# Kernel tuning notes

Measured on AMD Instinct MI355X. Metric: run time of the kernel, lower is better.

## Reference

```python
import jax, jax.numpy as jnp
import numpy as np

EPS = 1e-5
D_MODEL = 64
D_STATE = 16
D_INNER = 128  # expand=2
DT_RANK = 4    # ceil(64/16)


def _inorm(x):
    # InstanceNorm2d (affine=False), NCHW, biased variance, eps=1e-5
    mu = jnp.mean(x, axis=(2, 3), keepdims=True)
    var = jnp.var(x, axis=(2, 3), keepdims=True)
    return (x - mu) * jax.lax.rsqrt(var + EPS)


def _conv2d(x, w, b=None, groups=1):
    y = jax.lax.conv_general_dilated(x, w, (1, 1), 'SAME',
        dimension_numbers=('NCHW', 'OIHW', 'NCHW'), feature_group_count=groups)
    return y if b is None else y + b[None, :, None, None]


def _layernorm(x, w, b):
    mu = jnp.mean(x, axis=-1, keepdims=True)
    var = jnp.var(x, axis=-1, keepdims=True)
    return (x - mu) * jax.lax.rsqrt(var + EPS) * w + b


def _selective_scan(u, delta, A, Bm, Cm, Dp, delta_bias):
    # u, delta: (B,d,L); A: (d,N); Bm,Cm: (B,N,L); Dp: (d,)
    delta = jax.nn.softplus(delta + delta_bias[None, :, None])
    dA = jnp.exp(jnp.einsum('bdl,dn->lbdn', delta, A))        # (L,B,d,N)
    dBu = jnp.einsum('bdl,bnl->lbdn', delta * u, Bm)          # (L,B,d,N)
    Cl = jnp.transpose(Cm, (2, 0, 1))                         # (L,B,N)
    h0 = jnp.zeros((u.shape[0], u.shape[1], A.shape[1]), u.dtype)

    def step(h, inp):
        dA_l, dBu_l, c = inp
        h = dA_l * h + dBu_l
        return h, jnp.einsum('bdn,bn->bd', h, c)

    _, ys = jax.lax.scan(step, h0, (dA, dBu, Cl))             # ys: (L,B,d)
    return jnp.transpose(ys, (1, 2, 0)) + u * Dp[None, :, None]


def _forward(x, dw3_w, dw3_b, dw5_w, dw5_b, dw7_w, dw7_b, fuse_w, fuse_b,
             in_proj_w, conv2d_w, conv2d_b, x_proj_w, dt_proj_w, dt_proj_b,
             A_log, Dp, out_norm_w, out_norm_b, out_proj_w, cf_w, cf_b):
    C = x.shape[1]
    lrelu = lambda t: jax.nn.leaky_relu(t, 0.01)
    # ---- LRGS: multi-scale depthwise convs + fuse + residual (shortcut=Identity) ----
    feats = [lrelu(_inorm(_conv2d(x, w, b, groups=C)))
             for w, b in ((dw3_w, dw3_b), (dw5_w, dw5_b), (dw7_w, dw7_b))]
    xf = _conv2d(jnp.concatenate(feats, axis=1), fuse_w, fuse_b)
    x1 = lrelu(_inorm(xf)) + x
    # ---- MC_Mamba / SS2D ----
    xh = jnp.transpose(x1, (0, 2, 3, 1))           # (B,H,W,C)
    Bn, H, W, _ = xh.shape
    xz = xh @ in_proj_w.T                          # (B,H,W,2*d_inner)
    xm, z = jnp.split(xz, 2, axis=-1)
    xm = jnp.transpose(xm, (0, 3, 1, 2))           # (B,d_inner,H,W)
    xm = jax.nn.silu(_conv2d(xm, conv2d_w, conv2d_b, groups=D_INNER))
    L = H * W
    x_flat = jnp.transpose(xm.reshape(Bn, D_INNER, L), (0, 2, 1))  # (B,L,d)
    xp = x_flat @ x_proj_w.T
    dt, Bm, Cm = jnp.split(xp, [DT_RANK, DT_RANK + D_STATE], axis=-1)
    # NOTE: faithful to source, nn.Linear applies dt_proj_b here AND it is
    # passed again as delta_bias to the scan (bias applied twice).
    dt = jnp.transpose(dt @ dt_proj_w.T + dt_proj_b, (0, 2, 1))    # (B,d,L)
    A = -jnp.exp(A_log)
    y = _selective_scan(jnp.transpose(x_flat, (0, 2, 1)), dt, A,
                        jnp.transpose(Bm, (0, 2, 1)), jnp.transpose(Cm, (0, 2, 1)),
                        Dp, dt_proj_b)
    y = jnp.transpose(y, (0, 2, 1)).reshape(Bn, H, W, D_INNER)
    y = _layernorm(y, out_norm_w, out_norm_b) * jax.nn.silu(z)
    y = y @ out_proj_w.T                           # (B,H,W,d_model)
    y = jnp.transpose(y, (0, 3, 1, 2))
    y = _inorm(_conv2d(y, cf_w, cf_b))
    return x1 + y


def setup_inputs() -> dict:
    key = jax.random.key(0)
    ks = jax.random.split(key, 12)
    B, C, H, W = 8, D_MODEL, 64, 64
    s = 0.05
    return {
        'x': jax.random.normal(ks[0], (B, C, H, W), jnp.float32),
        'dw3_w': jax.random.normal(ks[1], (C, 1, 3, 3), jnp.float32) * s,
        'dw3_b': jnp.zeros((C,), jnp.float32),
        'dw5_w': jax.random.normal(ks[2], (C, 1, 5, 5), jnp.float32) * s,
        'dw5_b': jnp.zeros((C,), jnp.float32),
        'dw7_w': jax.random.normal(ks[3], (C, 1, 7, 7), jnp.float32) * s,
        'dw7_b': jnp.zeros((C,), jnp.float32),
        'fuse_w': jax.random.normal(ks[4], (C, 3 * C, 1, 1), jnp.float32) * s,
        'fuse_b': jnp.zeros((C,), jnp.float32),
        'in_proj_w': jax.random.normal(ks[5], (2 * D_INNER, D_MODEL), jnp.float32) * s,
        'conv2d_w': jax.random.normal(ks[6], (D_INNER, 1, 3, 3), jnp.float32) * s,
        'conv2d_b': jnp.zeros((D_INNER,), jnp.float32),
        'x_proj_w': jax.random.normal(ks[7], (DT_RANK + 2 * D_STATE, D_INNER), jnp.float32) * s,
        'dt_proj_w': jax.random.uniform(ks[8], (D_INNER, DT_RANK), jnp.float32, -0.5, 0.5),
        'dt_proj_b': jnp.exp(jax.random.uniform(ks[9], (D_INNER,), jnp.float32)
                             * (np.log(0.1) - np.log(0.001)) + np.log(0.001)).astype(jnp.float32),
        'A_log': jnp.log(jnp.tile(jnp.arange(1, D_STATE + 1, dtype=jnp.float32), (D_INNER, 1))),
        'Dp': jnp.ones((D_INNER,), jnp.float32),
        'out_norm_w': jnp.ones((D_INNER,), jnp.float32),
        'out_norm_b': jnp.zeros((D_INNER,), jnp.float32),
        'out_proj_w': jax.random.normal(ks[10], (D_MODEL, D_INNER), jnp.float32) * s,
        'cf_w': jax.random.normal(ks[11], (D_MODEL, D_MODEL, 1, 1), jnp.float32) * s,
        'cf_b': jnp.zeros((D_MODEL,), jnp.float32),
    }


def reference(x, dw3_w, dw3_b, dw5_w, dw5_b, dw7_w, dw7_b, fuse_w, fuse_b,
              in_proj_w, conv2d_w, conv2d_b, x_proj_w, dt_proj_w, dt_proj_b,
              A_log, Dp, out_norm_w, out_norm_b, out_proj_w, cf_w, cf_b):
    return _forward(x, dw3_w, dw3_b, dw5_w, dw5_b, dw7_w, dw7_b, fuse_w, fuse_b,
                    in_proj_w, conv2d_w, conv2d_b, x_proj_w, dt_proj_w, dt_proj_b,
                    A_log, Dp, out_norm_w, out_norm_b, out_proj_w, cf_w, cf_b)
```

## Files before the change

kernel.cpp:

```cpp
#include <hip/hip_runtime.h>
#include <math.h>

#define NB 8
#define NC 64
#define NL 4096
#define NDI 128
#define NN 16
#define CHUNK 32
#define NKCH 128

#define OFF_FEATS 0ull
#define OFF_AC    0ull
#define OFF_BC    2097152ull
#define OFF_HINIT 4194304ull
#define OFF_XF    6291456ull
#define OFF_BMAT  6291456ull
#define OFF_CMAT  6815744ull
#define OFF_X1    8388608ull
#define OFF_XMRAW 10485760ull
#define OFF_G     10485760ull
#define OFF_Z     14680064ull
#define OFF_YC    14680064ull
#define OFF_PART  16777216ull
#define OFF_STATS 16809984ull
#define OFF_XMC   18874368ull
#define OFF_DTM   23068672ull
#define OFF_SEGP  23199744ull
#define OFF_SEGQ  23330816ull
#define OFF_SEGH  23461888ull
#define OFF_WF    27262976ull
#define OFF_NSTAT (OFF_WF + 55552ull)
#define OFF_WCOMB (OFF_WF + 58624ull)
#define WS_NEED_FLOATS (OFF_WF + 66816ull)

#define WF_DW3    0
#define WF_DW5    576
#define WF_DW7    2176
#define WF_B3     5312
#define WF_B5     5376
#define WF_B7     5440
#define WF_FUSE   5504
#define WF_FUSEB  17792
#define WF_C2W    17856
#define WF_C2B    19008
#define WF_XPW    19136
#define WF_DTW    23744
#define WF_DTB    24256
#define WF_A      24384
#define WF_DP     26432
#define WF_ONW    26560
#define WF_ONB    26688
#define WF_OPW    26816
#define WF_CFW    35008
#define WF_CFB    39104
#define WF_INPJ   39168

struct Cvt { const float* src; float* dst; int n; int op; };
struct CvtArgs { Cvt d[22]; int ncvt; const float* cfw; const float* opw; float* wcomb; };

__global__ __launch_bounds__(256) void k0_cvt(CvtArgs a){
  if ((int)blockIdx.x < a.ncvt){
    Cvt c = a.d[blockIdx.x];
    for (int i = threadIdx.x; i < c.n; i += 256){
      float v = c.src[i];
      c.dst[i] = c.op ? -expf(v) : v;
    }
  } else {
    int idx = (blockIdx.x - a.ncvt)*256 + threadIdx.x;
    int c = idx >> 7, kk = idx & 127;
    float s = 0.f;
    #pragma unroll
    for (int j=0;j<64;j++) s += a.cfw[c*64+j] * a.opw[j*128+kk];
    a.wcomb[idx] = s;
  }
}

__global__ __launch_bounds__(256) void k1_dw(const float* __restrict__ x, const float* __restrict__ wf,
                                             float* __restrict__ feats, float* __restrict__ part){
  const int half = blockIdx.x & 1, c = (blockIdx.x >> 1) & 63, b = blockIdx.x >> 7;
  const int tid = threadIdx.x;
  const int r0 = half*32;
  __shared__ float xs[38*73];
  __shared__ float red[4][6];
  for (int i = tid; i < 38*73; i += 256) xs[i] = 0.f;
  const float* xp = x + ((size_t)b*64 + c)*NL;
  float v[10];
  #pragma unroll
  for (int k=0;k<10;k++){
    int idx = tid + k*256;
    int j = idx >> 6, w = idx & 63;
    int gr = r0 - 3 + j;
    bool ok = (idx < 2432) && (gr >= 0) && (gr < 64);
    v[k] = ok ? xp[gr*64 + w] : 0.f;
  }
  float w3r[9], w5r[25], w7r[49];
  #pragma unroll
  for (int i=0;i<9;i++)  w3r[i] = wf[WF_DW3 + c*9 + i];
  #pragma unroll
  for (int i=0;i<25;i++) w5r[i] = wf[WF_DW5 + c*25 + i];
  #pragma unroll
  for (int i=0;i<49;i++) w7r[i] = wf[WF_DW7 + c*49 + i];
  float b3 = wf[WF_B3+c], b5 = wf[WF_B5+c], b7 = wf[WF_B7+c];
  __syncthreads();
  #pragma unroll
  for (int k=0;k<10;k++){
    int idx = tid + k*256;
    if (idx < 2432){
      int j = idx >> 6, w = idx & 63;
      xs[j*73 + (w+3)] = v[k];
    }
  }
  __syncthreads();
  float s3=0,q3=0,s5=0,q5=0,s7=0,q7=0;
  float* f3 = feats + ((size_t)b*192 + c) * NL + r0*64;
  float* f5 = f3 + (size_t)64*NL;
  float* f7 = f3 + (size_t)128*NL;
  #pragma unroll
  for (int g=0; g<2; g++){
    int p = g*1024 + tid*4;
    int lh = p >> 6, w0 = p & 63;
    float a3[4], a5[4], a7[4];
    #pragma unroll
    for (int i=0;i<4;i++){ a3[i]=b3; a5[i]=b5; a7[i]=b7; }
    #pragma unroll
    for (int dy=0; dy<7; dy++){
      float s[10];
      #pragma unroll
      for (int j=0;j<10;j++) s[j] = xs[(lh+dy)*73 + w0 + j];
      #pragma unroll
      for (int dx=0;dx<7;dx++){
        float wv = w7r[dy*7+dx];
        #pragma unroll
        for (int i=0;i<4;i++) a7[i] += s[dx+i]*wv;
      }
      if (dy>=1 && dy<=5){
        #pragma unroll
        for (int dx=0;dx<5;dx++){
          float wv = w5r[(dy-1)*5+dx];
          #pragma unroll
          for (int i=0;i<4;i++) a5[i] += s[dx+1+i]*wv;
        }
      }
      if (dy>=2 && dy<=4){
        #pragma unroll
        for (int dx=0;dx<3;dx++){
          float wv = w3r[(dy-2)*3+dx];
          #pragma unroll
          for (int i=0;i<4;i++) a3[i] += s[dx+2+i]*wv;
        }
      }
    }
    *(float4*)(f3+p) = make_float4(a3[0],a3[1],a3[2],a3[3]);
    *(float4*)(f5+p) = make_float4(a5[0],a5[1],a5[2],a5[3]);
    *(float4*)(f7+p) = make_float4(a7[0],a7[1],a7[2],a7[3]);
    #pragma unroll
    for (int i=0;i<4;i++){
      s3+=a3[i]; q3+=a3[i]*a3[i];
      s5+=a5[i]; q5+=a5[i]*a5[i];
      s7+=a7[i]; q7+=a7[i]*a7[i];
    }
  }
  int wid = tid>>6, lane = tid&63;
  float v6[6]={s3,q3,s5,q5,s7,q7};
  #pragma unroll
  for (int j=0;j<6;j++){
    float t = v6[j];
    #pragma unroll
    for (int o=32;o>0;o>>=1) t += __shfl_down(t,o);
    if (!lane) red[wid][j]=t;
  }
  __syncthreads();
  if (tid < 3){
    float su = red[0][tid*2]+red[1][tid*2]+red[2][tid*2]+red[3][tid*2];
    float sq = red[0][tid*2+1]+red[1][tid*2+1]+red[2][tid*2+1]+red[3][tid*2+1];
    size_t k = (size_t)(b*192 + tid*64 + c)*4 + half*2;
    part[k]   = su;
    part[k+1] = sq;
  }
}

__global__ __launch_bounds__(256) void k2_fuse(const float* __restrict__ feats, const float* __restrict__ npart,
                                               const float* __restrict__ wf, float* __restrict__ xf){
  int og = blockIdx.x >> 8, rem = blockIdx.x & 255;
  int b = rem >> 5, pt = rem & 31;
  int jslot = threadIdx.x >> 5, pxslot = threadIdx.x & 31;
  __shared__ float wlds2[192][44];
  __shared__ float xs[32][128];
  __shared__ float msl[192], rsl[192];
  for (int i = threadIdx.x; i < 192; i += 256){
    const float* pp = npart + (size_t)(b*192+i)*4;
    float su = pp[0]+pp[2], sq = pp[1]+pp[3];
    float m = su*(1.f/NL);
    msl[i] = m;
    rsl[i] = rsqrtf(sq*(1.f/NL) - m*m + 1e-5f);
  }
  {
    const float* Wg = wf + WF_FUSE + og*32*192;
    for (int i = threadIdx.x; i < 6144; i += 256){
      int o = i / 192, k = i % 192;
      wlds2[k][o] = Wg[i];
    }
  }
  float acc[4][4];
  #pragma unroll
  for (int j=0;j<4;j++)
    #pragma unroll
    for (int p=0;p<4;p++) acc[j][p]=0.f;
  const float* fbase = feats + (size_t)b*192*NL + pt*128;
  for (int ch = 0; ch < 6; ch++){
    __syncthreads();
    for (int i = threadIdx.x; i < 1024; i += 256){
      int r = i >> 5, c4 = i & 31;
      int k = ch*32 + r;
      float4 f = *(const float4*)(fbase + (size_t)k*NL + c4*4);
      float m = msl[k], rs = rsl[k];
      float v0=(f.x-m)*rs, v1=(f.y-m)*rs, v2=(f.z-m)*rs, v3=(f.w-m)*rs;
      v0 = v0>0.f?v0:0.01f*v0; v1 = v1>0.f?v1:0.01f*v1;
      v2 = v2>0.f?v2:0.01f*v2; v3 = v3>0.f?v3:0.01f*v3;
      ((float4*)&xs[r][0])[c4] = make_float4(v0,v1,v2,v3);
    }
    __syncthreads();
    #pragma unroll 1
    for (int c = 0; c < 32; c++){
      float a[4];
      #pragma unroll
      for (int p=0;p<4;p++) a[p] = xs[c][pxslot + 32*p];
      float4 w4 = *(const float4*)&wlds2[ch*32+c][jslot*4];
      float wv[4] = {w4.x, w4.y, w4.z, w4.w};
      #pragma unroll
      for (int jj=0;jj<4;jj++)
        #pragma unroll
        for (int p=0;p<4;p++) acc[jj][p] += wv[jj]*a[p];
    }
  }
  #pragma unroll
  for (int jj=0;jj<4;jj++){
    int o = og*32 + jslot*4 + jj;
    float bias = wf[WF_FUSEB + o];
    float* dp = xf + (size_t)b*64*NL + (size_t)o*NL + pt*128;
    #pragma unroll
    for (int p=0;p<4;p++) dp[pxslot + 32*p] = acc[jj][p] + bias;
  }
}

__global__ __launch_bounds__(256) void k3_norm(const float* __restrict__ xf, const float* __restrict__ x,
                                               float* __restrict__ x1){
  const int tid = threadIdx.x;
  const size_t base = (size_t)blockIdx.x * NL;
  float loc[16]; float s=0.f, q=0.f;
  #pragma unroll
  for (int i=0;i<16;i++){ float v = xf[base + tid + i*256]; loc[i]=v; s+=v; q+=v*v; }
  __shared__ float red[4][2];
  int wid = tid>>6, lane = tid&63;
  #pragma unroll
  for (int o=32;o>0;o>>=1){ s += __shfl_down(s,o); q += __shfl_down(q,o); }
  if (!lane){ red[wid][0]=s; red[wid][1]=q; }
  __syncthreads();
  s = red[0][0]+red[1][0]+red[2][0]+red[3][0];
  q = red[0][1]+red[1][1]+red[2][1]+red[3][1];
  float m = s*(1.f/NL), va = q*(1.f/NL)-m*m, rs = rsqrtf(va+1e-5f);
  #pragma unroll
  for (int i=0;i<16;i++){
    int idx = tid + i*256;
    float v = (loc[i]-m)*rs;
    v = v>0.f ? v : 0.01f*v;
    x1[base+idx] = v + x[base+idx];
  }
}

__global__ __launch_bounds__(256) void k4_inproj(const float* __restrict__ x1, const float* __restrict__ wf,
                                                 float* __restrict__ xmraw, float* __restrict__ z){
  int og = blockIdx.x >> 8, rem = blockIdx.x & 255;
  int b = rem >> 5, pt = rem & 31;
  int jslot = threadIdx.x >> 5, pxslot = threadIdx.x & 31;
  __shared__ float wlds2[64][76];
  __shared__ float xs[32][128];
  {
    const float* Wg = wf + WF_INPJ + og*64*64;
    for (int i = threadIdx.x; i < 4096; i += 256){
      int o = i >> 6, k = i & 63;
      wlds2[k][o] = Wg[i];
    }
  }
  float acc[8][4];
  #pragma unroll
  for (int j=0;j<8;j++)
    #pragma unroll
    for (int p=0;p<4;p++) acc[j][p]=0.f;
  const float* xbase = x1 + (size_t)b*64*NL + pt*128;
  for (int ch = 0; ch < 2; ch++){
    __syncthreads();
    for (int i = threadIdx.x; i < 1024; i += 256){
      int r = i >> 5, c4 = i & 31;
      ((float4*)&xs[r][0])[c4] = *(const float4*)(xbase + (size_t)(ch*32+r)*NL + c4*4);
    }
    __syncthreads();
    #pragma unroll 1
    for (int c = 0; c < 32; c++){
      float a[4];
      #pragma unroll
      for (int p=0;p<4;p++) a[p] = xs[c][pxslot + 32*p];
      const float4* wp = (const float4*)&wlds2[ch*32+c][jslot*8];
      float4 w0 = wp[0], w1 = wp[1];
      float wv[8] = {w0.x,w0.y,w0.z,w0.w, w1.x,w1.y,w1.z,w1.w};
      #pragma unroll
      for (int jj=0;jj<8;jj++)
        #pragma unroll
        for (int p=0;p<4;p++) acc[jj][p] += wv[jj]*a[p];
    }
  }
  float* dstbase = (og < 2 ? xmraw + (size_t)b*128*NL + (size_t)(og*64)*NL
                           : z     + (size_t)b*128*NL + (size_t)((og-2)*64)*NL) + pt*128;
  #pragma unroll
  for (int jj=0;jj<8;jj++){
    float* dp = dstbase + (size_t)(jslot*8+jj)*NL;
    #pragma unroll
    for (int p=0;p<4;p++) dp[pxslot + 32*p] = acc[jj][p];
  }
}

__global__ __launch_bounds__(256) void k5_dw3(const float* __restrict__ xmraw, const float* __restrict__ wf,
                                              float* __restrict__ xmc){
  const int d = blockIdx.x & 127;
  const int tid = threadIdx.x;
  __shared__ float xs[66*69];
  for (int i=tid;i<66*69;i+=256) xs[i]=0.f;
  const float* xp = xmraw + (size_t)blockIdx.x * NL;
  float v[16];
  #pragma unroll
  for (int k=0;k<16;k++) v[k] = xp[tid + k*256];
  float wr[9];
  #pragma unroll
  for (int i=0;i<9;i++) wr[i] = wf[WF_C2W + d*9 + i];
  float bb = wf[WF_C2B + d];
  __syncthreads();
  #pragma unroll
  for (int k=0;k<16;k++){
    int i = tid + k*256;
    int h = i>>6, w = i&63;
    xs[(h+1)*69 + (w+1)] = v[k];
  }
  __syncthreads();
  float* op = xmc + (size_t)blockIdx.x * NL;
  #pragma unroll
  for (int g=0; g<4; g++){
    int p = g*1024 + tid*4;
    int h = p>>6, w0 = p&63;
    float a[4];
    #pragma unroll
    for (int i=0;i<4;i++) a[i]=bb;
    #pragma unroll
    for (int dy=0; dy<3; dy++){
      float s[6];
      #pragma unroll
      for (int j=0;j<6;j++) s[j] = xs[(h+dy)*69 + w0 + j];
      #pragma unroll
      for (int dx=0;dx<3;dx++){
        float wv = wr[dy*3+dx];
        #pragma unroll
        for (int i=0;i<4;i++) a[i] += s[dx+i]*wv;
      }
    }
    float4 o;
    o.x = a[0]/(1.f+__expf(-a[0]));
    o.y = a[1]/(1.f+__expf(-a[1]));
    o.z = a[2]/(1.f+__expf(-a[2]));
    o.w = a[3]/(1.f+__expf(-a[3]));
    *(float4*)(op+p) = o;
  }
}

__global__ __launch_bounds__(256) void k6_xproj(const float* __restrict__ xmc, const float* __restrict__ wf,
                                                float* __restrict__ Bm, float* __restrict__ Cm,
                                                float* __restrict__ dtm){
  int b = blockIdx.x >> 5, pt = blockIdx.x & 31;
  int jslot = threadIdx.x >> 6, pxslot = threadIdx.x & 63;
  __shared__ float wlds2[128][52];
  __shared__ float xs[32][128];
  {
    const float* Wg = wf + WF_XPW;
    for (int i = threadIdx.x; i < 4608; i += 256){
      int o = i >> 7, k = i & 127;
      wlds2[k][(o/9)*12 + (o%9)] = Wg[i];
    }
  }
  float acc[9][2];
  #pragma unroll
  for (int j=0;j<9;j++){ acc[j][0]=0.f; acc[j][1]=0.f; }
  const float* ubase = xmc + (size_t)b*128*NL + pt*128;
  for (int ch = 0; ch < 4; ch++){
    __syncthreads();
    for (int i = threadIdx.x; i < 1024; i += 256){
      int r = i >> 5, c4 = i & 31;
      ((float4*)&xs[r][0])[c4] = *(const float4*)(ubase + (size_t)(ch*32+r)*NL + c4*4);
    }
    __syncthreads();
    #pragma unroll 1
    for (int c = 0; c < 32; c++){
      float a0 = xs[c][pxslot];
      float a1 = xs[c][pxslot + 64];
      const float* wr = &wlds2[ch*32+c][jslot*12];
      float4 wa = *(const float4*)wr;
      float4 wb = *(const float4*)(wr+4);
      float w8 = wr[8];
      float wv[9] = {wa.x,wa.y,wa.z,wa.w, wb.x,wb.y,wb.z,wb.w, w8};
      #pragma unroll
      for (int j=0;j<9;j++){
        acc[j][0] += wv[j]*a0;
        acc[j][1] += wv[j]*a1;
      }
    }
  }
  #pragma unroll
  for (int j=0;j<9;j++){
    int o = jslot*9 + j;
    float* dp;
    if (o < 4)       dp = dtm + ((size_t)b*4 + o)*NL;
    else if (o < 20) dp = Bm  + ((size_t)b*16 + (o-4))*NL;
    else             dp = Cm  + ((size_t)b*16 + (o-20))*NL;
    dp[pt*128 + pxslot]      = acc[j][0];
    dp[pt*128 + pxslot + 64] = acc[j][1];
  }
}

__global__ __launch_bounds__(128) void k7_scan1(const float* __restrict__ xmc, const float* __restrict__ Bm,
                                                const float* __restrict__ dtm, const float* __restrict__ wf,
                                                float* __restrict__ Ac, float* __restrict__ Bc){
  int k = blockIdx.x & (NKCH-1), b = blockIdx.x >> 7;
  int d = threadIdx.x;
  int l0 = k*CHUNK;
  __shared__ float xs[128*33];
  __shared__ float Bl2[32*20];
  __shared__ float dtl2[32*4];
  float vx[32], vb[4], vd;
  #pragma unroll
  for (int j=0;j<32;j++){
    int i = d + 128*j;
    int ch = i >> 5, px = i & 31;
    vx[j] = xmc[((size_t)b*128+ch)*NL + l0 + px];
  }
  #pragma unroll
  for (int j=0;j<4;j++){
    int i = d + 128*j;
    int n = i >> 5, li = i & 31;
    vb[j] = Bm[((size_t)b*16+n)*NL + l0 + li];
  }
  { int n = d >> 5, li = d & 31; vd = dtm[((size_t)b*4+n)*NL + l0 + li]; }
  #pragma unroll
  for (int j=0;j<32;j++){
    int i = d + 128*j;
    int ch = i >> 5, px = i & 31;
    xs[ch*33+px] = vx[j];
  }
  #pragma unroll
  for (int j=0;j<4;j++){
    int i = d + 128*j;
    int n = i >> 5, li = i & 31;
    Bl2[li*20+n] = vb[j];
  }
  { int n = d >> 5, li = d & 31; dtl2[li*4+n] = vd; }
  float A[16], P[16], Q[16];
  const float* Af = wf + WF_A + d*16;
  #pragma unroll
  for (int n=0;n<16;n++){ A[n]=Af[n]; P[n]=1.f; Q[n]=0.f; }
  float w0 = wf[WF_DTW+d*4], w1 = wf[WF_DTW+d*4+1], w2 = wf[WF_DTW+d*4+2], w3 = wf[WF_DTW+d*4+3];
  float db2 = 2.f*wf[WF_DTB+d];
  __syncthreads();
  for (int l=0; l<CHUNK; l++){
    float4 dt4 = ((const float4*)dtl2)[l];
    float tt = w0*dt4.x + w1*dt4.y + w2*dt4.z + w3*dt4.w + db2;
    float de = tt > 20.f ? tt : __logf(1.f+__expf(tt));
    float du = de * xs[d*33+l];
    const float4* bp = (const float4*)(Bl2 + l*20);
    float4 b0 = bp[0], b1 = bp[1], b2 = bp[2], b3 = bp[3];
    float bb[16] = {b0.x,b0.y,b0.z,b0.w, b1.x,b1.y,b1.z,b1.w,
                    b2.x,b2.y,b2.z,b2.w, b3.x,b3.y,b3.z,b3.w};
    #pragma unroll
    for (int n=0;n<16;n++){
      float a = __expf(de*A[n]);
      P[n] *= a;
      Q[n] = a*Q[n] + du*bb[n];
    }
  }
  size_t base = (((size_t)k*NB + b)*128 + d)*16;
  #pragma unroll
  for (int i=0;i<4;i++){
    ((float4*)(Ac+base))[i] = make_float4(P[i*4],P[i*4+1],P[i*4+2],P[i*4+3]);
    ((float4*)(Bc+base))[i] = make_float4(Q[i*4],Q[i*4+1],Q[i*4+2],Q[i*4+3]);
  }
}

__global__ __launch_bounds__(256) void k8a_seg(const float* __restrict__ Ac, const float* __restrict__ Bc,
                                               float* __restrict__ segP, float* __restrict__ segQ){
  int idx = (blockIdx.x & 63)*256 + threadIdx.x;
  int seg = blockIdx.x >> 6;
  float av[16], bv[16];
  #pragma unroll
  for (int j=0;j<16;j++){
    size_t o = (size_t)(seg*16+j)*16384 + idx;
    av[j]=Ac[o]; bv[j]=Bc[o];
  }
  float P = 1.f, Q = 0.f;
  #pragma unroll
  for (int j=0;j<16;j++){ Q = av[j]*Q + bv[j]; P *= av[j]; }
  segP[seg*16384+idx]=P; segQ[seg*16384+idx]=Q;
}

__global__ __launch_bounds__(256) void k8b_mid(const float* __restrict__ segP, const float* __restrict__ segQ,
                                               float* __restrict__ segH){
  int idx = blockIdx.x*256 + threadIdx.x;
  float p[8], q[8];
  #pragma unroll
  for (int s=0;s<8;s++){ p[s]=segP[s*16384+idx]; q[s]=segQ[s*16384+idx]; }
  float h = 0.f;
  #pragma unroll
  for (int s=0;s<8;s++){ segH[s*16384+idx]=h; h = p[s]*h + q[s]; }
}

__global__ __launch_bounds__(256) void k8c_emit(const float* __restrict__ Ac, const float* __restrict__ Bc,
                                                const float* __restrict__ segH, float* __restrict__ Hi){
  int idx = (blockIdx.x & 63)*256 + threadIdx.x;
  int seg = blockIdx.x >> 6;
  float av[16], bv[16];
  #pragma unroll
  for (int j=0;j<16;j++){
    size_t o = (size_t)(seg*16+j)*16384 + idx;
    av[j]=Ac[o]; bv[j]=Bc[o];
  }
  float h = segH[seg*16384+idx];
  #pragma unroll
  for (int j=0;j<16;j++){
    size_t o = (size_t)(seg*16+j)*16384 + idx;
    Hi[o] = h;
    h = av[j]*h + bv[j];
  }
}

__global__ __launch_bounds__(128) void k9_scan2(const float* __restrict__ xmc, const float* __restrict__ Bm,
                                                const float* __restrict__ Cm, const float* __restrict__ dtm,
                                                const float* __restrict__ z, const float* __restrict__ wf,
                                                const float* __restrict__ Hi, float* __restrict__ G){
  int k = blockIdx.x & (NKCH-1), b = blockIdx.x >> 7;
  int d = threadIdx.x;
  int l0 = k*CHUNK;
  __shared__ float xs[128*33];
  __shared__ float Bl2[32*20], Cl2[32*20];
  __shared__ float dtl2[32*4];
  __shared__ float red[4][32][2];
  __shared__ float mstat[32], rstat[32];
  float vx[32], vb[4], vc[4], vd;
  #pragma unroll
  for (int j=0;j<32;j++){
    int i = d + 128*j;
    int ch = i >> 5, px = i & 31;
    vx[j] = xmc[((size_t)b*128+ch)*NL + l0 + px];
  }
  #pragma unroll
  for (int j=0;j<4;j++){
    int i = d + 128*j;
    int n = i >> 5, li = i & 31;
    vb[j] = Bm[((size_t)b*16+n)*NL + l0 + li];
    vc[j] = Cm[((size_t)b*16+n)*NL + l0 + li];
  }
  { int n = d >> 5, li = d & 31; vd = dtm[((size_t)b*4+n)*NL + l0 + li]; }
  float A[16], h[16];
  const float* Af = wf + WF_A + d*16;
  size_t hb = (((size_t)k*NB + b)*128 + d)*16;
  #pragma unroll
  for (int n=0;n<16;n++){ A[n]=Af[n]; h[n]=Hi[hb+n]; }
  #pragma unroll
  for (int j=0;j<32;j++){
    int i = d + 128*j;
    int ch = i >> 5, px = i & 31;
    xs[ch*33+px] = vx[j];
  }
  #pragma unroll
  for (int j=0;j<4;j++){
    int i = d + 128*j;
    int n = i >> 5, li = i & 31;
    Bl2[li*20+n] = vb[j];
    Cl2[li*20+n] = vc[j];
  }
  { int n = d >> 5, li = d & 31; dtl2[li*4+n] = vd; }
  float Dv = wf[WF_DP + d];
  float w0 = wf[WF_DTW+d*4], w1 = wf[WF_DTW+d*4+1], w2 = wf[WF_DTW+d*4+2], w3 = wf[WF_DTW+d*4+3];
  float db2 = 2.f*wf[WF_DTB+d];
  __syncthreads();
  for (int l=0; l<CHUNK; l++){
    float4 dt4 = ((const float4*)dtl2)[l];
    float tt = w0*dt4.x + w1*dt4.y + w2*dt4.z + w3*dt4.w + db2;
    float de = tt > 20.f ? tt : __logf(1.f+__expf(tt));
    float uu = xs[d*33+l];
    float du = de * uu;
    float yv = uu * Dv;
    const float4* bp = (const float4*)(Bl2 + l*20);
    const float4* cp = (const float4*)(Cl2 + l*20);
    float4 b0 = bp[0], b1 = bp[1], b2 = bp[2], b3 = bp[3];
    float4 c0 = cp[0], c1 = cp[1], c2 = cp[2], c3 = cp[3];
    float bb[16] = {b0.x,b0.y,b0.z,b0.w, b1.x,b1.y,b1.z,b1.w,
                    b2.x,b2.y,b2.z,b2.w, b3.x,b3.y,b3.z,b3.w};
    float cc[16] = {c0.x,c0.y,c0.z,c0.w, c1.x,c1.y,c1.z,c1.w,
                    c2.x,c2.y,c2.z,c2.w, c3.x,c3.y,c3.z,c3.w};
    #pragma unroll
    for (int n=0;n<16;n++){
      float a = __expf(de*A[n]);
      h[n] = a*h[n] + du*bb[n];
      yv  += h[n]*cc[n];
    }
    xs[d*33+l] = yv;
  }
  __syncthreads();
  {
    int px = d & 31, q = d >> 5;
    float s=0.f, qq=0.f;
    #pragma unroll
    for (int j=0;j<32;j++){ float v = xs[(q*32+j)*33+px]; s+=v; qq+=v*v; }
    red[q][px][0]=s; red[q][px][1]=qq;
  }
  __syncthreads();
  if (d < 32){
    float ss = red[0][d][0]+red[1][d][0]+red[2][d][0]+red[3][d][0];
    float sq = red[0][d][1]+red[1][d][1]+red[2][d][1]+red[3][d][1];
    float m = ss*(1.f/128.f);
    mstat[d] = m;
    rstat[d] = rsqrtf(sq*(1.f/128.f) - m*m + 1e-5f);
  }
  __syncthreads();
  float ow = wf[WF_ONW+d], ob = wf[WF_ONB+d];
  const float* zp = z + ((size_t)b*128+d)*NL + l0;
  float* gp = G + ((size_t)b*128+d)*NL + l0;
  #pragma unroll
  for (int l4=0; l4<CHUNK/4; l4++){
    float4 zv4 = ((const float4*)zp)[l4];
    float zv[4] = {zv4.x, zv4.y, zv4.z, zv4.w};
    float out[4];
    #pragma unroll
    for (int j=0;j<4;j++){
      int l = l4*4+j;
      float t = (xs[d*33+l]-mstat[l])*rstat[l]*ow + ob;
      out[j] = t * (zv[j]/(1.f+__expf(-zv[j])));
    }
    ((float4*)gp)[l4] = make_float4(out[0],out[1],out[2],out[3]);
  }
}

__global__ __launch_bounds__(256) void k11A_proj(const float* __restrict__ G, const float* __restrict__ wf,
                                                 const float* __restrict__ wcomb,
                                                 float* __restrict__ yc, float* __restrict__ part){
  int og = blockIdx.x >> 8, rem = blockIdx.x & 255;
  int b = rem >> 5, pt = rem & 31;
  int jslot = threadIdx.x >> 5, pxslot = threadIdx.x & 31;
  __shared__ float wlds2[128][44];
  __shared__ float xs[32][128];
  {
    const float* Wg = wcomb + og*32*128;
    for (int i = threadIdx.x; i < 4096; i += 256){
      int o = i >> 7, k = i & 127;
      wlds2[k][o] = Wg[i];
    }
  }
  float acc[4][4];
  #pragma unroll
  for (int j=0;j<4;j++)
    #pragma unroll
    for (int p=0;p<4;p++) acc[j][p]=0.f;
  const float* gbase = G + (size_t)b*128*NL + pt*128;
  for (int ch = 0; ch < 4; ch++){
    __syncthreads();
    for (int i = threadIdx.x; i < 1024; i += 256){
      int r = i >> 5, c4 = i & 31;
      ((float4*)&xs[r][0])[c4] = *(const float4*)(gbase + (size_t)(ch*32+r)*NL + c4*4);
    }
    __syncthreads();
    #pragma unroll 1
    for (int c = 0; c < 32; c++){
      float a[4];
      #pragma unroll
      for (int p=0;p<4;p++) a[p] = xs[c][pxslot + 32*p];
      float4 w4 = *(const float4*)&wlds2[ch*32+c][jslot*4];
      float wv[4] = {w4.x, w4.y, w4.z, w4.w};
      #pragma unroll
      for (int jj=0;jj<4;jj++)
        #pragma unroll
        for (int p=0;p<4;p++) acc[jj][p] += wv[jj]*a[p];
    }
  }
  #pragma unroll
  for (int jj=0;jj<4;jj++){
    int cc = og*32 + jslot*4 + jj;
    float bias = wf[WF_CFB + cc];
    float* dp = yc + (size_t)b*64*NL + (size_t)cc*NL + pt*128;
    float sv = 0.f, qv = 0.f;
    #pragma unroll
    for (int p=0;p<4;p++){
      float t = acc[jj][p] + bias;
      dp[pxslot + 32*p] = t;
      sv += t; qv += t*t;
    }
    #pragma unroll
    for (int o=16;o>0;o>>=1){ sv += __shfl_xor(sv,o); qv += __shfl_xor(qv,o); }
    if (pxslot == 0){
      size_t pidx = (((size_t)b*64 + cc)*32 + pt)*2;
      part[pidx] = sv; part[pidx+1] = qv;
    }
  }
}

__global__ __launch_bounds__(256) void k11b_stats(const float* __restrict__ part, float* __restrict__ stats){
  int i = blockIdx.x*256 + threadIdx.x;
  if (i >= 512) return;
  float s=0.f, q=0.f;
  #pragma unroll
  for (int t2=0;t2<32;t2++){ s += part[((size_t)i*32+t2)*2]; q += part[((size_t)i*32+t2)*2+1]; }
  float m = s*(1.f/NL), va = q*(1.f/NL) - m*m;
  stats[i*2] = m; stats[i*2+1] = rsqrtf(va+1e-5f);
}

__global__ __launch_bounds__(256) void k11c_final(const float* __restrict__ yc, const float* __restrict__ stats,
                                                  const float* __restrict__ x1, float* __restrict__ out){
  int bc = blockIdx.x;
  float m = stats[bc*2], rs = stats[bc*2+1];
  size_t base = (size_t)bc*NL;
  for (int i=threadIdx.x;i<NL;i+=256){
    float v = (yc[base+i]-m)*rs;
    out[base+i] = x1[base+i] + v;
  }
}

extern "C" void kernel_launch(void* const* d_in, const int* in_sizes, int n_in,
                              void* d_out, int out_size, void* d_ws, size_t ws_size,
                              hipStream_t stream) {
  if (ws_size < WS_NEED_FLOATS * sizeof(float)) return;
  const float* x     = (const float*)d_in[0];
  const float* dw3w  = (const float*)d_in[1];
  const float* dw3b  = (const float*)d_in[2];
  const float* dw5w  = (const float*)d_in[3];
  const float* dw5b  = (const float*)d_in[4];
  const float* dw7w  = (const float*)d_in[5];
  const float* dw7b  = (const float*)d_in[6];
  const float* fusew = (const float*)d_in[7];
  const float* fuseb = (const float*)d_in[8];
  const float* inpjw = (const float*)d_in[9];
  const float* c2w   = (const float*)d_in[10];
  const float* c2b   = (const float*)d_in[11];
  const float* xpw   = (const float*)d_in[12];
  const float* dtw   = (const float*)d_in[13];
  const float* dtb   = (const float*)d_in[14];
  const float* alog  = (const float*)d_in[15];
  const float* dpv   = (const float*)d_in[16];
  const float* onw   = (const float*)d_in[17];
  const float* onb   = (const float*)d_in[18];
  const float* opw   = (const float*)d_in[19];
  const float* cfw   = (const float*)d_in[20];
  const float* cfb   = (const float*)d_in[21];

  float* ws    = (float*)d_ws;
  float* wf    = ws + OFF_WF;
  float* wcomb = ws + OFF_WCOMB;
  float* feats = ws + OFF_FEATS;
  float* xf    = ws + OFF_XF;
  float* x1    = ws + OFF_X1;
  float* xmraw = ws + OFF_XMRAW;
  float* z     = ws + OFF_Z;
  float* xmc   = ws + OFF_XMC;
  float* Bmw   = ws + OFF_BMAT;
  float* Cmw   = ws + OFF_CMAT;
  float* dtm   = ws + OFF_DTM;
  float* Acb   = ws + OFF_AC;
  float* Bcb   = ws + OFF_BC;
  float* Hi    = ws + OFF_HINIT;
  float* segP  = ws + OFF_SEGP;
  float* segQ  = ws + OFF_SEGQ;
  float* segH  = ws + OFF_SEGH;
  float* G     = ws + OFF_G;
  float* yc    = ws + OFF_YC;
  float* part  = ws + OFF_PART;
  float* stats = ws + OFF_STATS;

  CvtArgs ca; int ns = 0;
  auto add = [&](const float* s, int off, int n, int op){
    ca.d[ns].src = s; ca.d[ns].dst = wf + off; ca.d[ns].n = n; ca.d[ns].op = op; ns++;
  };
  add(dw3w, WF_DW3, 576, 0);   add(dw5w, WF_DW5, 1600, 0);  add(dw7w, WF_DW7, 3136, 0);
  add(dw3b, WF_B3, 64, 0);     add(dw5b, WF_B5, 64, 0);     add(dw7b, WF_B7, 64, 0);
  add(fusew, WF_FUSE, 12288, 0); add(fuseb, WF_FUSEB, 64, 0);
  add(c2w, WF_C2W, 1152, 0);   add(c2b, WF_C2B, 128, 0);
  add(xpw, WF_XPW, 4608, 0);   add(dtw, WF_DTW, 512, 0);    add(dtb, WF_DTB, 128, 0);
  add(alog, WF_A, 2048, 1);
  add(dpv, WF_DP, 128, 0);
  add(onw, WF_ONW, 128, 0);    add(onb, WF_ONB, 128, 0);
  add(opw, WF_OPW, 8192, 0);
  add(cfw, WF_CFW, 4096, 0);   add(cfb, WF_CFB, 64, 0);
  add(inpjw, WF_INPJ, 16384, 0);
  ca.ncvt = ns; ca.cfw = cfw; ca.opw = opw; ca.wcomb = wcomb;

  k0_cvt<<<ns + 32, 256, 0, stream>>>(ca);
  k1_dw<<<1024, 256, 0, stream>>>(x, wf, feats, part);
  k2_fuse<<<512, 256, 0, stream>>>(feats, part, wf, xf);
  k3_norm<<<512, 256, 0, stream>>>(xf, x, x1);
  k4_inproj<<<1024, 256, 0, stream>>>(x1, wf, xmraw, z);
  k5_dw3<<<1024, 256, 0, stream>>>(xmraw, wf, xmc);
  k6_xproj<<<256, 256, 0, stream>>>(xmc, wf, Bmw, Cmw, dtm);
  k7_scan1<<<1024, 128, 0, stream>>>(xmc, Bmw, dtm, wf, Acb, Bcb);
  k8a_seg<<<512, 256, 0, stream>>>(Acb, Bcb, segP, segQ);
  k8b_mid<<<64, 256, 0, stream>>>(segP, segQ, segH);
  k8c_emit<<<512, 256, 0, stream>>>(Acb, Bcb, segH, Hi);
  k9_scan2<<<1024, 128, 0, stream>>>(xmc, Bmw, Cmw, dtm, z, wf, Hi, G);
  k11A_proj<<<512, 256, 0, stream>>>(G, wf, wcomb, yc, part);
  k11b_stats<<<2, 256, 0, stream>>>(part, stats);
  k11c_final<<<512, 256, 0, stream>>>(yc, stats, x1, (float*)d_out);
}
```

Before: 212.7 us.

## Split depthwise conv grids finer and merge scan-carry and stats kernels

The multi-scale depthwise conv kernel now splits each channel into four row bands instead of two, and the 3x3 conv kernel into two halves instead of whole planes. This doubles the block count for more parallelism, at the cost of extra halo loads. The three-kernel segmented carry propagation across chunks is collapsed into one sequential kernel with 64 blocks. The final stats kernel is folded into the output kernel, so each block reduces its own partial sums. Together these cut kernel launches, but the merged carry kernel runs 128 serial steps on fewer blocks.

Result: no change. 209.9 us (-1.3%).

```diff
diff --git a/kernel.cpp b/kernel.cpp
--- a/kernel.cpp
+++ b/kernel.cpp
@@ -25,9 +25,6 @@
 #define OFF_STATS 16809984ull
 #define OFF_XMC   18874368ull
 #define OFF_DTM   23068672ull
-#define OFF_SEGP  23199744ull
-#define OFF_SEGQ  23330816ull
-#define OFF_SEGH  23461888ull
 #define OFF_WF    27262976ull
 #define OFF_NSTAT (OFF_WF + 55552ull)
 #define OFF_WCOMB (OFF_WF + 58624ull)
@@ -77,20 +74,20 @@
 
 __global__ __launch_bounds__(256) void k1_dw(const float* __restrict__ x, const float* __restrict__ wf,
                                              float* __restrict__ feats, float* __restrict__ part){
-  const int half = blockIdx.x & 1, c = (blockIdx.x >> 1) & 63, b = blockIdx.x >> 7;
+  const int quar = blockIdx.x & 3, c = (blockIdx.x >> 2) & 63, b = blockIdx.x >> 8;
   const int tid = threadIdx.x;
-  const int r0 = half*32;
-  __shared__ float xs[38*73];
+  const int r0 = quar*16;
+  __shared__ float xs[22*73];
   __shared__ float red[4][6];
-  for (int i = tid; i < 38*73; i += 256) xs[i] = 0.f;
+  for (int i = tid; i < 22*73; i += 256) xs[i] = 0.f;
   const float* xp = x + ((size_t)b*64 + c)*NL;
-  float v[10];
-  #pragma unroll
-  for (int k=0;k<10;k++){
+  float v[6];
+  #pragma unroll
+  for (int k=0;k<6;k++){
     int idx = tid + k*256;
     int j = idx >> 6, w = idx & 63;
     int gr = r0 - 3 + j;
-    bool ok = (idx < 2432) && (gr >= 0) && (gr < 64);
+    bool ok = (idx < 1408) && (gr >= 0) && (gr < 64);
     v[k] = ok ? xp[gr*64 + w] : 0.f;
   }
   float w3r[9], w5r[25], w7r[49];
@@ -103,9 +100,9 @@
   float b3 = wf[WF_B3+c], b5 = wf[WF_B5+c], b7 = wf[WF_B7+c];
   __syncthreads();
   #pragma unroll
-  for (int k=0;k<10;k++){
+  for (int k=0;k<6;k++){
     int idx = tid + k*256;
-    if (idx < 2432){
+    if (idx < 1408){
       int j = idx >> 6, w = idx & 63;
       xs[j*73 + (w+3)] = v[k];
     }
@@ -115,9 +112,8 @@
   float* f3 = feats + ((size_t)b*192 + c) * NL + r0*64;
   float* f5 = f3 + (size_t)64*NL;
   float* f7 = f3 + (size_t)128*NL;
-  #pragma unroll
-  for (int g=0; g<2; g++){
-    int p = g*1024 + tid*4;
+  {
+    int p = tid*4;
     int lh = p >> 6, w0 = p & 63;
     float a3[4], a5[4], a7[4];
     #pragma unroll
@@ -173,7 +169,7 @@
   if (tid < 3){
     float su = red[0][tid*2]+red[1][tid*2]+red[2][tid*2]+red[3][tid*2];
     float sq = red[0][tid*2+1]+red[1][tid*2+1]+red[2][tid*2+1]+red[3][tid*2+1];
-    size_t k = (size_t)(b*192 + tid*64 + c)*4 + half*2;
+    size_t k = (size_t)(b*192 + tid*64 + c)*8 + quar*2;
     part[k]   = su;
     part[k+1] = sq;
   }
@@ -188,8 +184,8 @@
   __shared__ float xs[32][128];
   __shared__ float msl[192], rsl[192];
   for (int i = threadIdx.x; i < 192; i += 256){
-    const float* pp = npart + (size_t)(b*192+i)*4;
-    float su = pp[0]+pp[2], sq = pp[1]+pp[3];
+    const float* pp = npart + (size_t)(b*192+i)*8;
+    float su = pp[0]+pp[2]+pp[4]+pp[6], sq = pp[1]+pp[3]+pp[5]+pp[7];
     float m = su*(1.f/NL);
     msl[i] = m;
     rsl[i] = rsqrtf(sq*(1.f/NL) - m*m + 1e-5f);
@@ -321,31 +317,42 @@
 
 __global__ __launch_bounds__(256) void k5_dw3(const float* __restrict__ xmraw, const float* __restrict__ wf,
                                               float* __restrict__ xmc){
-  const int d = blockIdx.x & 127;
+  const int half = blockIdx.x & 1;
+  const int d = (blockIdx.x >> 1) & 127;
+  const int bd = blockIdx.x >> 1;
   const int tid = threadIdx.x;
-  __shared__ float xs[66*69];
-  for (int i=tid;i<66*69;i+=256) xs[i]=0.f;
-  const float* xp = xmraw + (size_t)blockIdx.x * NL;
-  float v[16];
-  #pragma unroll
-  for (int k=0;k<16;k++) v[k] = xp[tid + k*256];
+  const int r0 = half*32;
+  __shared__ float xs[34*69];
+  for (int i=tid;i<34*69;i+=256) xs[i]=0.f;
+  const float* xp = xmraw + (size_t)bd * NL;
+  float v[9];
+  #pragma unroll
+  for (int k=0;k<9;k++){
+    int idx = tid + k*256;
+    int j = idx >> 6, w = idx & 63;
+    int gr = r0 - 1 + j;
+    bool ok = (idx < 2176) && (gr >= 0) && (gr < 64);
+    v[k] = ok ? xp[gr*64 + w] : 0.f;
+  }
   float wr[9];
   #pragma unroll
   for (int i=0;i<9;i++) wr[i] = wf[WF_C2W + d*9 + i];
   float bb = wf[WF_C2B + d];
   __syncthreads();
   #pragma unroll
-  for (int k=0;k<16;k++){
-    int i = tid + k*256;
-    int h = i>>6, w = i&63;
-    xs[(h+1)*69 + (w+1)] = v[k];
-  }
-  __syncthreads();
-  float* op = xmc + (size_t)blockIdx.x * NL;
-  #pragma unroll
-  for (int g=0; g<4; g++){
+  for (int k=0;k<9;k++){
+    int idx = tid + k*256;
+    if (idx < 2176){
+      int j = idx >> 6, w = idx & 63;
+      xs[j*69 + (w+1)] = v[k];
+    }
+  }
+  __syncthreads();
+  float* op = xmc + (size_t)bd * NL + r0*64;
+  #pragma unroll
+  for (int g=0; g<2; g++){
     int p = g*1024 + tid*4;
-    int h = p>>6, w0 = p&63;
+    int lh = p>>6, w0 = p&63;
     float a[4];
     #pragma unroll
     for (int i=0;i<4;i++) a[i]=bb;
@@ -353,7 +360,7 @@
     for (int dy=0; dy<3; dy++){
       float s[6];
       #pragma unroll
-      for (int j=0;j<6;j++) s[j] = xs[(h+dy)*69 + w0 + j];
+      for (int j=0;j<6;j++) s[j] = xs[(lh+dy)*69 + w0 + j];
       #pragma unroll
       for (int dx=0;dx<3;dx++){
         float wv = wr[dy*3+dx];
@@ -490,49 +497,23 @@
   }
 }
 
-__global__ __launch_bounds__(256) void k8a_seg(const float* __restrict__ Ac, const float* __restrict__ Bc,
-                                               float* __restrict__ segP, float* __restrict__ segQ){
-  int idx = (blockIdx.x & 63)*256 + threadIdx.x;
-  int seg = blockIdx.x >> 6;
-  float av[16], bv[16];
-  #pragma unroll
-  for (int j=0;j<16;j++){
-    size_t o = (size_t)(seg*16+j)*16384 + idx;
-    av[j]=Ac[o]; bv[j]=Bc[o];
-  }
-  float P = 1.f, Q = 0.f;
-  #pragma unroll
-  for (int j=0;j<16;j++){ Q = av[j]*Q + bv[j]; P *= av[j]; }
-  segP[seg*16384+idx]=P; segQ[seg*16384+idx]=Q;
-}
-
-__global__ __launch_bounds__(256) void k8b_mid(const float* __restrict__ segP, const float* __restrict__ segQ,
-                                               float* __restrict__ segH){
+__global__ __launch_bounds__(256) void k8_mid(const float* __restrict__ Ac, const float* __restrict__ Bc,
+                                              float* __restrict__ Hi){
   int idx = blockIdx.x*256 + threadIdx.x;
-  float p[8], q[8];
-  #pragma unroll
-  for (int s=0;s<8;s++){ p[s]=segP[s*16384+idx]; q[s]=segQ[s*16384+idx]; }
   float h = 0.f;
-  #pragma unroll
-  for (int s=0;s<8;s++){ segH[s*16384+idx]=h; h = p[s]*h + q[s]; }
-}
-
-__global__ __launch_bounds__(256) void k8c_emit(const float* __restrict__ Ac, const float* __restrict__ Bc,
-                                                const float* __restrict__ segH, float* __restrict__ Hi){
-  int idx = (blockIdx.x & 63)*256 + threadIdx.x;
-  int seg = blockIdx.x >> 6;
-  float av[16], bv[16];
-  #pragma unroll
-  for (int j=0;j<16;j++){
-    size_t o = (size_t)(seg*16+j)*16384 + idx;
-    av[j]=Ac[o]; bv[j]=Bc[o];
-  }
-  float h = segH[seg*16384+idx];
-  #pragma unroll
-  for (int j=0;j<16;j++){
-    size_t o = (size_t)(seg*16+j)*16384 + idx;
-    Hi[o] = h;
-    h = av[j]*h + bv[j];
+  for (int k0=0;k0<NKCH;k0+=16){
+    float av[16], bv[16];
+    #pragma unroll
+    for (int j=0;j<16;j++){
+      size_t o = (size_t)(k0+j)*16384 + idx;
+      av[j]=Ac[o]; bv[j]=Bc[o];
+    }
+    #pragma unroll
+    for (int j=0;j<16;j++){
+      size_t o = (size_t)(k0+j)*16384 + idx;
+      Hi[o] = h;
+      h = av[j]*h + bv[j];
+    }
   }
 }
 
@@ -706,20 +687,19 @@
   }
 }
 
-__global__ __launch_bounds__(256) void k11b_stats(const float* __restrict__ part, float* __restrict__ stats){
-  int i = blockIdx.x*256 + threadIdx.x;
-  if (i >= 512) return;
-  float s=0.f, q=0.f;
-  #pragma unroll
-  for (int t2=0;t2<32;t2++){ s += part[((size_t)i*32+t2)*2]; q += part[((size_t)i*32+t2)*2+1]; }
-  float m = s*(1.f/NL), va = q*(1.f/NL) - m*m;
-  stats[i*2] = m; stats[i*2+1] = rsqrtf(va+1e-5f);
-}
-
-__global__ __launch_bounds__(256) void k11c_final(const float* __restrict__ yc, const float* __restrict__ stats,
+__global__ __launch_bounds__(256) void k11c_final(const float* __restrict__ yc, const float* __restrict__ part,
                                                   const float* __restrict__ x1, float* __restrict__ out){
   int bc = blockIdx.x;
-  float m = stats[bc*2], rs = stats[bc*2+1];
+  __shared__ float sm, sr;
+  if (threadIdx.x == 0){
+    float s=0.f, q=0.f;
+    #pragma unroll
+    for (int t2=0;t2<32;t2++){ s += part[((size_t)bc*32+t2)*2]; q += part[((size_t)bc*32+t2)*2+1]; }
+    float m = s*(1.f/NL);
+    sm = m; sr = rsqrtf(q*(1.f/NL) - m*m + 1e-5f);
+  }
+  __syncthreads();
+  float m = sm, rs = sr;
   size_t base = (size_t)bc*NL;
   for (int i=threadIdx.x;i<NL;i+=256){
     float v = (yc[base+i]-m)*rs;
@@ -769,13 +749,9 @@
   float* Acb   = ws + OFF_AC;
   float* Bcb   = ws + OFF_BC;
   float* Hi    = ws + OFF_HINIT;
-  float* segP  = ws + OFF_SEGP;
-  float* segQ  = ws + OFF_SEGQ;
-  float* segH  = ws + OFF_SEGH;
   float* G     = ws + OFF_G;
   float* yc    = ws + OFF_YC;
   float* part  = ws + OFF_PART;
-  float* stats = ws + OFF_STATS;
 
   CvtArgs ca; int ns = 0;
   auto add = [&](const float* s, int off, int n, int op){
@@ -795,18 +771,15 @@
   ca.ncvt = ns; ca.cfw = cfw; ca.opw = opw; ca.wcomb = wcomb;
 
   k0_cvt<<<ns + 32, 256, 0, stream>>>(ca);
-  k1_dw<<<1024, 256, 0, stream>>>(x, wf, feats, part);
+  k1_dw<<<2048, 256, 0, stream>>>(x, wf, feats, part);
   k2_fuse<<<512, 256, 0, stream>>>(feats, part, wf, xf);
   k3_norm<<<512, 256, 0, stream>>>(xf, x, x1);
   k4_inproj<<<1024, 256, 0, stream>>>(x1, wf, xmraw, z);
-  k5_dw3<<<1024, 256, 0, stream>>>(xmraw, wf, xmc);
+  k5_dw3<<<2048, 256, 0, stream>>>(xmraw, wf, xmc);
   k6_xproj<<<256, 256, 0, stream>>>(xmc, wf, Bmw, Cmw, dtm);
   k7_scan1<<<1024, 128, 0, stream>>>(xmc, Bmw, dtm, wf, Acb, Bcb);
-  k8a_seg<<<512, 256, 0, stream>>>(Acb, Bcb, segP, segQ);
-  k8b_mid<<<64, 256, 0, stream>>>(segP, segQ, segH);
-  k8c_emit<<<512, 256, 0, stream>>>(Acb, Bcb, segH, Hi);
+  k8_mid<<<64, 256, 0, stream>>>(Acb, Bcb, Hi);
   k9_scan2<<<1024, 128, 0, stream>>>(xmc, Bmw, Cmw, dtm, z, wf, Hi, G);
   k11A_proj<<<512, 256, 0, stream>>>(G, wf, wcomb, yc, part);
-  k11b_stats<<<2, 256, 0, stream>>>(part, stats);
-  k11c_final<<<512, 256, 0, stream>>>(yc, stats, x1, (float*)d_out);
-}
+  k11c_final<<<512, 256, 0, stream>>>(yc, part, x1, (float*)d_out);
+}
```
